# Kernel optimization log

Measured on AMD Instinct MI355X. Metric: run time of the kernel, lower is better.

The kernel has to match this reference:

```python
import jax, jax.numpy as jnp
import numpy as np

D = 512   # Nsites: single-particle Hilbert space dimension
N = 128   # Nparticles
TINY = 1e-30


def setup_inputs() -> dict:
    key = jax.random.key(0)
    k1, k2 = jax.random.split(key)
    # Orthonormal orbitals (mirrors reortho_orbitals: QR of a random matrix)
    A = jax.random.normal(k1, (D, D), dtype=jnp.float32)
    Q, _ = jnp.linalg.qr(A)
    P = Q[:, :N]                                   # (D, N) orthonormal columns
    u = jax.random.uniform(k2, (N,), dtype=jnp.float32)  # inverse-CDF draws, one per particle
    return {"P": P, "u": u}


def _sample(P, u):
    """Ordered componentwise sampling from the Slater determinant.

    Uses the identity that Ksites is always a contiguous range [0..i], so the
    determinant ratios -det(G[0:i+1]-diag(occ+e_i))/det(G[0:x_{k-1}+1]-diag(occ))
    reduce to running products of Schur-complement pivots s_j = G_jj - b^T Xinv b
    of the leading block of (G - diag(occ)).  A single O(D) scan maintains the
    (padded) inverse of that leading block via rank-1 bordered-inverse updates,
    replacing the per-step np.ix_/vstack/det kernel launches of the original.
    """
    dt = P.dtype
    G = jnp.eye(D, dtype=dt) - P @ P.T             # (D, D), symmetric projection complement
    idxs = jnp.arange(D)

    def step(carry, i):
        Xinv, ratio, cumul, k = carry
        b = jnp.where(idxs < i, G[:, i], 0.0)      # border column, masked to leading block
        v = Xinv @ b                               # Xinv is zero-padded beyond processed block
        s = G[i, i] - b @ v                        # Schur pivot (site i unoccupied)
        last_allowed = D - N + k                   # xmax - 1 for particle k
        active = (k < N) & (i <= last_allowed)
        # cond prob particle k sits at site i: -(s-1) * prod of unoccupied pivots since x_{k-1}
        p = jnp.where(active, -(s - 1.0) * ratio, 0.0)
        u_k = u[jnp.clip(k, 0, N - 1)]
        occupy = active & ((cumul + p >= u_k) | (i == last_allowed))  # inverse-CDF; force at support end
        pivot = jnp.where(occupy, s - 1.0, s)
        pivot = jnp.where(jnp.abs(pivot) < TINY, TINY, pivot)
        # bordered inverse update: [[X,b],[b,d]]^-1 via outer(vext,vext)/pivot
        vext = jnp.where(idxs == i, -1.0, v)
        Xinv = Xinv + jnp.outer(vext, vext) / pivot
        ratio = jnp.where(occupy, 1.0, jnp.where(active, ratio * s, ratio))
        cumul = jnp.where(occupy, 0.0, cumul + p)
        k = k + occupy.astype(jnp.int32)
        return (Xinv, ratio, cumul, k), (p, k - occupy.astype(jnp.int32), occupy)

    init = (jnp.zeros((D, D), dtype=dt), jnp.asarray(1.0, dt), jnp.asarray(0.0, dt),
            jnp.asarray(0, jnp.int32))
    _, (p_rec, k_rec, occ_rec) = jax.lax.scan(step, init, idxs)

    krow = jnp.where(k_rec < N, k_rec, N)          # out-of-range rows dropped
    cond_probs = jnp.zeros((N, D), dtype=dt).at[krow, idxs].set(p_rec, mode='drop')
    return cond_probs, occ_rec


def reference(P, u):
    cond_probs, occ = _sample(P, u)
    positions = jnp.nonzero(occ, size=N, fill_value=-1)[0]  # ordered sampled sites
    return cond_probs, positions
```

## Files before the change

### kernel.cpp

```cpp
#include <hip/hip_runtime.h>


#define DD 512
#define NN 128
#define NTHREADS 512
#define BB 16
#define NBLK (DD / BB)

typedef float v2f __attribute__((ext_vector_type(2)));

__device__ __forceinline__ float lane_bcast(float v, int l) {
  return __int_as_float(__builtin_amdgcn_readlane(__float_as_int(v), l));
}
__device__ __forceinline__ void pk_fma_vv(v2f& acc, v2f a, v2f b) {
  asm("v_pk_fma_f32 %0, %1, %2, %0" : "+v"(acc) : "v"(a), "v"(b));
}
__device__ __forceinline__ void pk_fma_vs(v2f& acc, v2f a, v2f bs) {
  asm("v_pk_fma_f32 %0, %1, %2, %0" : "+v"(acc) : "v"(a), "s"(bs));
}
__device__ __forceinline__ v2f pk_mul_vv(v2f a, v2f b) {
  v2f d;
  asm("v_pk_mul_f32 %0, %1, %2" : "=v"(d) : "v"(a), "v"(b));
  return d;
}
__device__ __forceinline__ void pk_add_vv(v2f& acc, v2f a) {
  asm("v_pk_add_f32 %0, %1, %0" : "+v"(acc) : "v"(a));
}

__device__ __forceinline__ float wave_reduce_add64(float sd) {
#if __has_builtin(__builtin_amdgcn_permlane32_swap)
  {
    unsigned xi = __float_as_uint(sd);
    auto r = __builtin_amdgcn_permlane32_swap(xi, xi, false, false);
    sd = __uint_as_float(r[0]) + __uint_as_float(r[1]);
  }
#else
  sd += __shfl_xor(sd, 32, 64);
#endif
#if __has_builtin(__builtin_amdgcn_permlane16_swap)
  {
    unsigned xi = __float_as_uint(sd);
    auto r = __builtin_amdgcn_permlane16_swap(xi, xi, false, false);
    sd = __uint_as_float(r[0]) + __uint_as_float(r[1]);
  }
#else
  sd += __shfl_xor(sd, 16, 64);
#endif
  sd += __int_as_float(
      __builtin_amdgcn_update_dpp(0, __float_as_int(sd), 0x128, 0xF, 0xF, true));
  sd += __int_as_float(
      __builtin_amdgcn_ds_swizzle(__float_as_int(sd), 0x101F));
  sd += __int_as_float(
      __builtin_amdgcn_update_dpp(0, __float_as_int(sd), 0x4E, 0xF, 0xF, true));
  sd += __int_as_float(
      __builtin_amdgcn_update_dpp(0, __float_as_int(sd), 0xB1, 0xF, 0xF, true));
  return sd;
}

__global__ __launch_bounds__(NTHREADS) void slater_scan_kernel(
    const float* __restrict__ P, const float* __restrict__ u,
    float* __restrict__ out) {
  const int tid   = threadIdx.x;
  const int wave  = tid >> 6;
  const int lane  = tid & 63;
  const int c0    = wave << 4;
  const int rbase = c0 & 63;
  const bool lowhalf = (wave < 4);

  __shared__ __align__(16) float part[8][64][36];
  __shared__ __align__(16) float VldT[16][129];
  __shared__ __align__(16) float Cld[16][20];
  __shared__ __align__(16) float Pst[2][BB][NN];

  for (int j = tid; j < NN * DD; j += NTHREADS) out[j] = 0.0f;

  const float ur0 = u[lane];
  const float ur1 = u[64 + lane];

  const int sr = tid >> 5;
  const int sc = (tid & 31) << 2;
  *(float4*)&Pst[0][sr][sc] = *(const float4*)&P[sr * NN + sc];

  v2f A2r0[8], A2r1[8];
#pragma unroll
  for (int jp = 0; jp < 8; ++jp) {
    A2r0[jp] = (v2f){(lane == c0 + 2 * jp) ? 1.0f : 0.0f,
                     (lane == c0 + 2 * jp + 1) ? 1.0f : 0.0f};
    A2r1[jp] = (v2f){(lane + 64 == c0 + 2 * jp) ? 1.0f : 0.0f,
                     (lane + 64 == c0 + 2 * jp + 1) ? 1.0f : 0.0f};
  }

  float ratio = 1.0f, cumul = 0.0f;
  int k = 0;

  __syncthreads();

  for (int blk = 0; blk < NBLK; ++blk) {
    const int i0  = blk * BB;
    const int buf = blk & 1;

    float4 stg;
    const bool do_stage = (blk + 1 < NBLK);
    if (do_stage) stg = *(const float4*)&P[(i0 + BB + sr) * NN + sc];

    const int t2 = 2 * wave;
    const float pt0l = Pst[buf][t2][lane];
    const float pt0h = Pst[buf][t2][64 + lane];
    const float pt1l = Pst[buf][t2 + 1][lane];
    const float pt1h = Pst[buf][t2 + 1][64 + lane];

    float pa0[16], pa1[16];
#pragma unroll
    for (int t = 0; t < 16; ++t) {
      const float4 q0 = *(const float4*)&Pst[buf][t][c0];
      const float4 q1 = *(const float4*)&Pst[buf][t][c0 + 4];
      const float4 q2 = *(const float4*)&Pst[buf][t][c0 + 8];
      const float4 q3 = *(const float4*)&Pst[buf][t][c0 + 12];
      const v2f pp0 = {q0.x, q0.y}, pp1 = {q0.z, q0.w};
      const v2f pp2 = {q1.x, q1.y}, pp3 = {q1.z, q1.w};
      const v2f pp4 = {q2.x, q2.y}, pp5 = {q2.z, q2.w};
      const v2f pp6 = {q3.x, q3.y}, pp7 = {q3.z, q3.w};
      v2f a0 = pk_mul_vv(A2r0[0], pp0);
      v2f a1 = pk_mul_vv(A2r1[0], pp0);
      pk_fma_vv(a0, A2r0[1], pp1); pk_fma_vv(a1, A2r1[1], pp1);
      pk_fma_vv(a0, A2r0[2], pp2); pk_fma_vv(a1, A2r1[2], pp2);
      pk_fma_vv(a0, A2r0[3], pp3); pk_fma_vv(a1, A2r1[3], pp3);
      pk_fma_vv(a0, A2r0[4], pp4); pk_fma_vv(a1, A2r1[4], pp4);
      pk_fma_vv(a0, A2r0[5], pp5); pk_fma_vv(a1, A2r1[5], pp5);
      pk_fma_vv(a0, A2r0[6], pp6); pk_fma_vv(a1, A2r1[6], pp6);
      pk_fma_vv(a0, A2r0[7], pp7); pk_fma_vv(a1, A2r1[7], pp7);
      pa0[t] = a0.x + a0.y;
      pa1[t] = a1.x + a1.y;
    }
    {
      float4* myp = (float4*)&part[wave][lane][0];
      myp[0] = make_float4(pa0[0],  pa0[1],  pa0[2],  pa0[3]);
      myp[1] = make_float4(pa0[4],  pa0[5],  pa0[6],  pa0[7]);
      myp[2] = make_float4(pa0[8],  pa0[9],  pa0[10], pa0[11]);
      myp[3] = make_float4(pa0[12], pa0[13], pa0[14], pa0[15]);
      myp[4] = make_float4(pa1[0],  pa1[1],  pa1[2],  pa1[3]);
      myp[5] = make_float4(pa1[4],  pa1[5],  pa1[6],  pa1[7]);
      myp[6] = make_float4(pa1[8],  pa1[9],  pa1[10], pa1[11]);
      myp[7] = make_float4(pa1[12], pa1[13], pa1[14], pa1[15]);
    }
    if (do_stage) *(float4*)&Pst[buf ^ 1][sr][sc] = stg;
    __syncthreads();

    {
      const int r  = tid >> 2;
      const int qd = tid & 3;
      const int rl = r & 63;
      const int rh = (r >> 6) << 4;
      v2f s01 = {0.0f, 0.0f}, s23 = {0.0f, 0.0f};
#pragma unroll
      for (int v = 0; v < 8; ++v) {
        const float4 x = *(const float4*)&part[v][rl][rh + 4 * qd];
        pk_add_vv(s01, (v2f){x.x, x.y});
        pk_add_vv(s23, (v2f){x.z, x.w});
      }
      VldT[4 * qd + 0][r] = s01.x;
      VldT[4 * qd + 1][r] = s01.y;
      VldT[4 * qd + 2][r] = s23.x;
      VldT[4 * qd + 3][r] = s23.y;
    }
    __syncthreads();

    v2f Wp[16];
#pragma unroll
    for (int m2 = 0; m2 < 16; ++m2)
      Wp[m2] = (v2f){VldT[m2][lane], VldT[m2][lane + 64]};

    {
      float cr0[16], cr1[16];
#pragma unroll
      for (int mm = 0; mm < 16; ++mm) {
        cr0[mm] = wave_reduce_add64(fmaf(pt0l, Wp[mm].x, pt0h * Wp[mm].y));
        cr1[mm] = wave_reduce_add64(fmaf(pt1l, Wp[mm].x, pt1h * Wp[mm].y));
      }
      if (lane == 0) {
        float4* cp0 = (float4*)&Cld[t2][0];
        cp0[0] = make_float4(cr0[0],  cr0[1],  cr0[2],  cr0[3]);
        cp0[1] = make_float4(cr0[4],  cr0[5],  cr0[6],  cr0[7]);
        cp0[2] = make_float4(cr0[8],  cr0[9],  cr0[10], cr0[11]);
        cp0[3] = make_float4(cr0[12], cr0[13], cr0[14], cr0[15]);
        float4* cp1 = (float4*)&Cld[t2 + 1][0];
        cp1[0] = make_float4(cr1[0],  cr1[1],  cr1[2],  cr1[3]);
        cp1[1] = make_float4(cr1[4],  cr1[5],  cr1[6],  cr1[7]);
        cp1[2] = make_float4(cr1[8],  cr1[9],  cr1[10], cr1[11]);
        cp1[3] = make_float4(cr1[12], cr1[13], cr1[14], cr1[15]);
      }
    }
    __syncthreads();

    const int m = lane & 15;
    float Cc[16];
#pragma unroll
    for (int t = 0; t < 16; ++t) Cc[t] = Cld[t][m];
    float qdiag = Cld[m][m];
    float Dreg[16], SD[16];
    v2f SWp[16];
    bool done = false;
#pragma unroll
    for (int t = 0; t < 16; ++t) {
      const float s = 1.0f - lane_bcast(qdiag, t);
      const int i = i0 + t;
      const int last_allowed = DD - NN + k;
      const bool active = (k < NN) && (i <= last_allowed);
      const float pr = active ? (-(s - 1.0f) * ratio) : 0.0f;
      const int kidx = (k < NN) ? k : (NN - 1);
      const float uk_l = lane_bcast(ur0, kidx & 63);
      const float uk_h = lane_bcast(ur1, kidx & 63);
      const float uk = (kidx < 64) ? uk_l : uk_h;
      const bool occupy = active && ((cumul + pr >= uk) || (i == last_allowed));
      float pivot = occupy ? (s - 1.0f) : s;
      pivot = (fabsf(pivot) < 1e-30f) ? 1e-30f : pivot;
      const float invp = 1.0f / pivot;

      if (tid == 0) {
        if (k < NN) out[k * DD + i] = pr;
        if (occupy) out[NN * DD + k] = (float)i;
      }

      ratio = occupy ? 1.0f : (active ? ratio * s : ratio);
      cumul = occupy ? 0.0f : (cumul + pr);
      k += occupy ? 1 : 0;
      if (k == NN) { done = true; break; }

      float d = Cc[t];
#pragma unroll
      for (int j = 0; j < t; ++j) {
        const float djt = lane_bcast(Dreg[j], t);
        d = fmaf(djt, SD[j], d);
        pk_fma_vs(Wp[t], SWp[j], (v2f){djt, djt});
      }
      Dreg[t] = d;
      SD[t]   = d * invp;
      SWp[t]  = pk_mul_vv(Wp[t], (v2f){invp, invp});
      qdiag   = fmaf(d, SD[t], qdiag);
    }
    if (done) return;

    {
      auto upd = [&](bool low) {
#pragma unroll
        for (int t = 0; t < 16; ++t) {
          const v2f w0d = {SWp[t].x, SWp[t].x};
          const v2f w1d = {SWp[t].y, SWp[t].y};
          const float wsrc = low ? Wp[t].x : Wp[t].y;
#pragma unroll
          for (int jp = 0; jp < 8; ++jp) {
            const v2f wc2 = {lane_bcast(wsrc, rbase + 2 * jp),
                             lane_bcast(wsrc, rbase + 2 * jp + 1)};
            pk_fma_vs(A2r0[jp], w0d, wc2);
            pk_fma_vs(A2r1[jp], w1d, wc2);
          }
        }
      };
      if (lowhalf) upd(true); else upd(false);
    }
  }
}

extern "C" void kernel_launch(void* const* d_in, const int* in_sizes, int n_in,
                              void* d_out, int out_size, void* d_ws,
                              size_t ws_size, hipStream_t stream) {
  const float* P = (const float*)d_in[0];
  const float* u = (const float*)d_in[1];
  float* out = (float*)d_out;
  hipLaunchKernelGGL(slater_scan_kernel, dim3(1), dim3(NTHREADS), 0, stream,
                     P, u, out);
}
```

Measured before the change: 464.2 us.

## Pack dual wave reductions, switch to right-looking block factorization, stage update columns in LDS

The two per-row wave reductions are merged into a single packed reduction so that shuffle and DPP steps work on v2f pairs. The in-block recurrence changes from left-looking (accumulate D from earlier columns) to right-looking: once a pivot is known, the remaining Ereg and Wp entries are updated right away, which shortens the dependency chain before each pivot is read. The rank-16 trailing update no longer takes 128 readlane broadcasts per wave. It stores the needed W column slice to a small LDS array and reads it back with float4 loads, which adds LDS traffic and a same-wave store-to-load dependency.

```diff
diff --git a/kernel.cpp b/kernel.cpp
--- a/kernel.cpp
+++ b/kernel.cpp
@@ -57,6 +57,56 @@
   return sd;
 }
 
+__device__ __forceinline__ v2f wave_reduce_add64_pk(v2f sd) {
+#if __has_builtin(__builtin_amdgcn_permlane32_swap)
+  {
+    unsigned xl = __float_as_uint(sd.x), xh = __float_as_uint(sd.y);
+    auto rl = __builtin_amdgcn_permlane32_swap(xl, xl, false, false);
+    auto rh = __builtin_amdgcn_permlane32_swap(xh, xh, false, false);
+    v2f partner = {__uint_as_float(rl[1]), __uint_as_float(rh[1])};
+    v2f self    = {__uint_as_float(rl[0]), __uint_as_float(rh[0])};
+    sd = self;
+    pk_add_vv(sd, partner);
+  }
+#else
+  sd.x += __shfl_xor(sd.x, 32, 64);
+  sd.y += __shfl_xor(sd.y, 32, 64);
+#endif
+#if __has_builtin(__builtin_amdgcn_permlane16_swap)
+  {
+    unsigned xl = __float_as_uint(sd.x), xh = __float_as_uint(sd.y);
+    auto rl = __builtin_amdgcn_permlane16_swap(xl, xl, false, false);
+    auto rh = __builtin_amdgcn_permlane16_swap(xh, xh, false, false);
+    v2f partner = {__uint_as_float(rl[1]), __uint_as_float(rh[1])};
+    v2f self    = {__uint_as_float(rl[0]), __uint_as_float(rh[0])};
+    sd = self;
+    pk_add_vv(sd, partner);
+  }
+#else
+  sd.x += __shfl_xor(sd.x, 16, 64);
+  sd.y += __shfl_xor(sd.y, 16, 64);
+#endif
+  sd.x += __int_as_float(__builtin_amdgcn_update_dpp(
+      0, __float_as_int(sd.x), 0x128, 0xF, 0xF, true));
+  sd.y += __int_as_float(__builtin_amdgcn_update_dpp(
+      0, __float_as_int(sd.y), 0x128, 0xF, 0xF, true));
+  {
+    v2f partner = {
+        __int_as_float(__builtin_amdgcn_ds_swizzle(__float_as_int(sd.x), 0x101F)),
+        __int_as_float(__builtin_amdgcn_ds_swizzle(__float_as_int(sd.y), 0x101F))};
+    pk_add_vv(sd, partner);
+  }
+  sd.x += __int_as_float(__builtin_amdgcn_update_dpp(
+      0, __float_as_int(sd.x), 0x4E, 0xF, 0xF, true));
+  sd.y += __int_as_float(__builtin_amdgcn_update_dpp(
+      0, __float_as_int(sd.y), 0x4E, 0xF, 0xF, true));
+  sd.x += __int_as_float(__builtin_amdgcn_update_dpp(
+      0, __float_as_int(sd.x), 0xB1, 0xF, 0xF, true));
+  sd.y += __int_as_float(__builtin_amdgcn_update_dpp(
+      0, __float_as_int(sd.y), 0xB1, 0xF, 0xF, true));
+  return sd;
+}
+
 __global__ __launch_bounds__(NTHREADS) void slater_scan_kernel(
     const float* __restrict__ P, const float* __restrict__ u,
     float* __restrict__ out) {
@@ -64,13 +114,13 @@
   const int wave  = tid >> 6;
   const int lane  = tid & 63;
   const int c0    = wave << 4;
-  const int rbase = c0 & 63;
   const bool lowhalf = (wave < 4);
 
   __shared__ __align__(16) float part[8][64][36];
   __shared__ __align__(16) float VldT[16][129];
   __shared__ __align__(16) float Cld[16][20];
   __shared__ __align__(16) float Pst[2][BB][NN];
+  __shared__ __align__(16) float Wst[8][16][20];
 
   for (int j = tid; j < NN * DD; j += NTHREADS) out[j] = 0.0f;
 
@@ -103,11 +153,11 @@
     const bool do_stage = (blk + 1 < NBLK);
     if (do_stage) stg = *(const float4*)&P[(i0 + BB + sr) * NN + sc];
 
-    const int t2 = 2 * wave;
-    const float pt0l = Pst[buf][t2][lane];
-    const float pt0h = Pst[buf][t2][64 + lane];
-    const float pt1l = Pst[buf][t2 + 1][lane];
-    const float pt1h = Pst[buf][t2 + 1][64 + lane];
+    const int t2r = 2 * wave;
+    const float pt0l = Pst[buf][t2r][lane];
+    const float pt0h = Pst[buf][t2r][64 + lane];
+    const float pt1l = Pst[buf][t2r + 1][lane];
+    const float pt1h = Pst[buf][t2r + 1][64 + lane];
 
     float pa0[16], pa1[16];
 #pragma unroll
@@ -171,38 +221,34 @@
       Wp[m2] = (v2f){VldT[m2][lane], VldT[m2][lane + 64]};
 
     {
-      float cr0[16], cr1[16];
+      v2f cr[16];
 #pragma unroll
       for (int mm = 0; mm < 16; ++mm) {
-        cr0[mm] = wave_reduce_add64(fmaf(pt0l, Wp[mm].x, pt0h * Wp[mm].y));
-        cr1[mm] = wave_reduce_add64(fmaf(pt1l, Wp[mm].x, pt1h * Wp[mm].y));
+        const v2f wx = {Wp[mm].x, Wp[mm].x};
+        const v2f wy = {Wp[mm].y, Wp[mm].y};
+        v2f seed = pk_mul_vv((v2f){pt0h, pt1h}, wy);
+        pk_fma_vv(seed, (v2f){pt0l, pt1l}, wx);
+        cr[mm] = wave_reduce_add64_pk(seed);
       }
       if (lane == 0) {
-        float4* cp0 = (float4*)&Cld[t2][0];
-        cp0[0] = make_float4(cr0[0],  cr0[1],  cr0[2],  cr0[3]);
-        cp0[1] = make_float4(cr0[4],  cr0[5],  cr0[6],  cr0[7]);
-        cp0[2] = make_float4(cr0[8],  cr0[9],  cr0[10], cr0[11]);
-        cp0[3] = make_float4(cr0[12], cr0[13], cr0[14], cr0[15]);
-        float4* cp1 = (float4*)&Cld[t2 + 1][0];
-        cp1[0] = make_float4(cr1[0],  cr1[1],  cr1[2],  cr1[3]);
-        cp1[1] = make_float4(cr1[4],  cr1[5],  cr1[6],  cr1[7]);
-        cp1[2] = make_float4(cr1[8],  cr1[9],  cr1[10], cr1[11]);
-        cp1[3] = make_float4(cr1[12], cr1[13], cr1[14], cr1[15]);
+#pragma unroll
+        for (int mm = 0; mm < 16; ++mm) {
+          Cld[t2r][mm]     = cr[mm].x;
+          Cld[t2r + 1][mm] = cr[mm].y;
+        }
       }
     }
     __syncthreads();
 
     const int m = lane & 15;
-    float Cc[16];
-#pragma unroll
-    for (int t = 0; t < 16; ++t) Cc[t] = Cld[t][m];
-    float qdiag = Cld[m][m];
-    float Dreg[16], SD[16];
+    float Ereg[16];
+#pragma unroll
+    for (int t = 0; t < 16; ++t) Ereg[t] = Cld[t][m];
     v2f SWp[16];
     bool done = false;
 #pragma unroll
     for (int t = 0; t < 16; ++t) {
-      const float s = 1.0f - lane_bcast(qdiag, t);
+      const float s = 1.0f - lane_bcast(Ereg[t], t);
       const int i = i0 + t;
       const int last_allowed = DD - NN + k;
       const bool active = (k < NN) && (i <= last_allowed);
@@ -226,37 +272,47 @@
       k += occupy ? 1 : 0;
       if (k == NN) { done = true; break; }
 
-      float d = Cc[t];
-#pragma unroll
-      for (int j = 0; j < t; ++j) {
-        const float djt = lane_bcast(Dreg[j], t);
-        d = fmaf(djt, SD[j], d);
-        pk_fma_vs(Wp[t], SWp[j], (v2f){djt, djt});
-      }
-      Dreg[t] = d;
-      SD[t]   = d * invp;
-      SWp[t]  = pk_mul_vv(Wp[t], (v2f){invp, invp});
-      qdiag   = fmaf(d, SD[t], qdiag);
+      const float SDl = Ereg[t] * invp;
+      SWp[t] = pk_mul_vv(Wp[t], (v2f){invp, invp});
+#pragma unroll
+      for (int t2 = t + 1; t2 < 16; ++t2) {
+        const float djt2 = lane_bcast(Ereg[t], t2);
+        Ereg[t2] = fmaf(djt2, SDl, Ereg[t2]);
+        pk_fma_vs(Wp[t2], SWp[t], (v2f){djt2, djt2});
+      }
     }
     if (done) return;
 
     {
-      auto upd = [&](bool low) {
-#pragma unroll
-        for (int t = 0; t < 16; ++t) {
-          const v2f w0d = {SWp[t].x, SWp[t].x};
-          const v2f w1d = {SWp[t].y, SWp[t].y};
-          const float wsrc = low ? Wp[t].x : Wp[t].y;
-#pragma unroll
-          for (int jp = 0; jp < 8; ++jp) {
-            const v2f wc2 = {lane_bcast(wsrc, rbase + 2 * jp),
-                             lane_bcast(wsrc, rbase + 2 * jp + 1)};
-            pk_fma_vs(A2r0[jp], w0d, wc2);
-            pk_fma_vs(A2r1[jp], w1d, wc2);
-          }
-        }
-      };
-      if (lowhalf) upd(true); else upd(false);
+      const bool writer = ((lane >> 4) == (wave & 3));
+      const int jl = lane & 15;
+      if (writer) {
+#pragma unroll
+        for (int t = 0; t < 16; ++t)
+          Wst[wave][t][jl] = lowhalf ? Wp[t].x : Wp[t].y;
+      }
+    }
+
+#pragma unroll
+    for (int t = 0; t < 16; ++t) {
+      const float4 q0 = *(const float4*)&Wst[wave][t][0];
+      const float4 q1 = *(const float4*)&Wst[wave][t][4];
+      const float4 q2 = *(const float4*)&Wst[wave][t][8];
+      const float4 q3 = *(const float4*)&Wst[wave][t][12];
+      const v2f w0d = {SWp[t].x, SWp[t].x};
+      const v2f w1d = {SWp[t].y, SWp[t].y};
+      const v2f c01 = {q0.x, q0.y}, c23 = {q0.z, q0.w};
+      const v2f c45 = {q1.x, q1.y}, c67 = {q1.z, q1.w};
+      const v2f c89 = {q2.x, q2.y}, cab = {q2.z, q2.w};
+      const v2f ccd = {q3.x, q3.y}, cef = {q3.z, q3.w};
+      pk_fma_vv(A2r0[0], w0d, c01); pk_fma_vv(A2r1[0], w1d, c01);
+      pk_fma_vv(A2r0[1], w0d, c23); pk_fma_vv(A2r1[1], w1d, c23);
+      pk_fma_vv(A2r0[2], w0d, c45); pk_fma_vv(A2r1[2], w1d, c45);
+      pk_fma_vv(A2r0[3], w0d, c67); pk_fma_vv(A2r1[3], w1d, c67);
+      pk_fma_vv(A2r0[4], w0d, c89); pk_fma_vv(A2r1[4], w1d, c89);
+      pk_fma_vv(A2r0[5], w0d, cab); pk_fma_vv(A2r1[5], w1d, cab);
+      pk_fma_vv(A2r0[6], w0d, ccd); pk_fma_vv(A2r1[6], w1d, ccd);
+      pk_fma_vv(A2r0[7], w0d, cef); pk_fma_vv(A2r1[7], w1d, cef);
     }
   }
 }
```

After: 425.7 us. 1.09x faster.
